# Performance work log

Measured on AMD Instinct MI355X. Metric: run time of the kernel, lower is better.

Reference implementation:

```python
import jax, jax.numpy as jnp
import numpy as np

N, E, H, NH, RBF_K = 512, 4096, 128, 8, 64
CUTOFF = 10.0
HH = H * NH  # 1024


def setup_inputs() -> dict:
    key = jax.random.key(0)
    ks = jax.random.split(key, 30)
    def lin_w(k, fan_in, fan_out):
        return jax.random.normal(k, (fan_in, fan_out), jnp.float32) * (fan_in ** -0.5)
    inp = {
        'atom_embs': jax.random.normal(ks[0], (N, H), jnp.float32),
        'pos': jax.random.normal(ks[1], (N, 3), jnp.float32),
        'edge_weight': jax.random.normal(ks[2], (E,), jnp.float32),
        'edge_indices': jax.random.randint(ks[3], (2, E), 0, N, jnp.int64),
        'Wq': lin_w(ks[4], H, HH),
        'Wk': lin_w(ks[5], H, HH),
        'Wv': lin_w(ks[6], H, HH),
        'li_w': lin_w(ks[7], H, H), 'li_b': jnp.zeros((H,), jnp.float32),
        'lj_w': lin_w(ks[8], H, H), 'lj_b': jnp.zeros((H,), jnp.float32),
        'el_w': lin_w(ks[9], 3 * H, HH), 'el_b': jnp.zeros((HH,), jnp.float32),
        'rl_w': lin_w(ks[10], RBF_K, HH), 'rl_b': jnp.zeros((HH,), jnp.float32),
        'ol_w': lin_w(ks[11], HH, H), 'ol_b': jnp.zeros((H,), jnp.float32),
        'ln_g': jnp.ones((H,), jnp.float32), 'ln_b': jnp.zeros((H,), jnp.float32),
        'f1_w': lin_w(ks[12], H, H), 'f1_b': jnp.zeros((H,), jnp.float32),
        'f2_w': lin_w(ks[13], H, H), 'f2_b': jnp.zeros((H,), jnp.float32),
        'f3_w': lin_w(ks[14], H, H), 'f3_b': jnp.zeros((H,), jnp.float32),
    }
    return inp


def _scatter_softmax_cols(logits, seg, num_segments):
    # softmax over columns of `logits` grouped by seg (column -> source node)
    lt = logits.T                                   # [E_cols, E_rows]
    m = jax.ops.segment_max(lt, seg, num_segments=num_segments)
    e = jnp.exp(lt - m[seg])
    s = jax.ops.segment_sum(e, seg, num_segments=num_segments)
    return (e / s[seg]).T


def _rbf(d):
    # d: [E, 1]. ExponentialRBF with softplus(softplus_inverse(x)) == x identities
    centers = jnp.linspace(1.0, np.exp(-CUTOFF).astype(np.float32), RBF_K)
    widths = np.float32((0.5 / ((1.0 - np.exp(-CUTOFF)) / RBF_K)) ** 2)
    x = d / CUTOFF
    x3 = x ** 3; x4 = x3 * x; x5 = x4 * x
    cut = jnp.where(x < 1, 1 - 6 * x5 + 15 * x4 - 10 * x3, jnp.zeros_like(x))
    return cut * jnp.exp(-widths * (jnp.exp(-d) - centers) ** 2)   # [E, K]


def reference(atom_embs, pos, edge_weight, edge_indices, Wq, Wk, Wv,
              li_w, li_b, lj_w, lj_b, el_w, el_b, rl_w, rl_b, ol_w, ol_b,
              ln_g, ln_b, f1_w, f1_b, f2_w, f2_b, f3_w, f3_b):
    src, tgt = edge_indices[0], edge_indices[1]
    ew = edge_weight[:, None]
    ai = atom_embs[tgt] + ew                      # atom_embs_i (+= edge_weight)
    aj = atom_embs[src] + ew                      # atom_embs_j (+= edge_weight)
    Q = ai @ Wq
    K = ai @ Wk
    V = ai @ Wv                                   # [E, HH]
    logits = (Q @ K.T) * (H ** -0.5)              # [E, E]
    prod = _scatter_softmax_cols(logits, src, N)  # scatter_softmax over edge_indices[0]
    hi = ai @ li_w + li_b
    hj = aj @ lj_w + lj_b
    edge_ij = jnp.concatenate([hi + hj, hi - hj, hi * hj], axis=-1)  # [E, 3H]
    d = jnp.linalg.norm(pos[tgt] - pos[src], axis=-1)[:, None]       # [E, 1]
    feats = edge_ij @ el_w + el_b + _rbf(d) @ rl_w + rl_b + V        # [E, HH]
    msg = (prod @ feats) @ ol_w + ol_b            # [E, H]
    agg = jax.ops.segment_sum(msg, tgt, num_segments=N)              # [N, H]

    def ln(x):
        mu = jnp.mean(x, -1, keepdims=True)
        var = jnp.var(x, -1, keepdims=True)
        return (x - mu) / jnp.sqrt(var + 1e-5) * ln_g + ln_b

    h = ln(agg)
    sp = jax.nn.softplus
    h = sp(sp(sp(h @ f1_w + f1_b) @ f2_w + f2_b) @ f3_w + f3_b)
    return ln(h)
```

## Files before the change

### kernel.cpp

```cpp
#include <hip/hip_runtime.h>
#include <math.h>

#define N_NODES 512
#define NE      4096
#define H       128
#define HH      1024
#define RBFK    64
#define KCAT    576
#define ALPHA   0.08838834764831845f

typedef __attribute__((ext_vector_type(8))) short bf16x8;
typedef __attribute__((ext_vector_type(4))) float f32x4;
typedef __attribute__((ext_vector_type(4))) short short4v;

__device__ __forceinline__ short f2bf(float x) {
    unsigned u = __builtin_bit_cast(unsigned, x);
    unsigned r = u + 0x7FFFu + ((u >> 16) & 1u);
    return (short)(r >> 16);
}
__device__ __forceinline__ float bf2f(short s) {
    return __builtin_bit_cast(float, ((unsigned)(unsigned short)s) << 16);
}

__device__ __forceinline__ void gload16(const short* g, short* l) {
    __builtin_amdgcn_global_load_lds(
        (const __attribute__((address_space(1))) void*)g,
        (__attribute__((address_space(3))) void*)l, 16, 0, 0);
}


__global__ __launch_bounds__(512) void k_sort(
    const int* __restrict__ ei, const float* __restrict__ ew,
    int* __restrict__ srcS, int* __restrict__ tgtS, float* __restrict__ ewS,
    int* __restrict__ idxT,
    int* __restrict__ segStart, int* __restrict__ segStartT,
    int* __restrict__ nsegp, float* __restrict__ cvec)
{
    __shared__ int hS[N_NODES], hT[N_NODES], sS[N_NODES], sT[N_NODES];
    __shared__ int flag;
    int t = threadIdx.x;
    if (t < 64) {
        int vv = ei[2 * t + 1];
        unsigned long long m = __ballot(vv != 0);
        if (t == 0) flag = (m == 0ULL);
    }
    hS[t] = 0; hT[t] = 0;
    if (t < H) cvec[t] = 0.0f;
    __syncthreads();
    int is64 = flag;
    for (int e = t; e < NE; e += 512) {
        int s = is64 ? ei[2 * e]          : ei[e];
        int g = is64 ? ei[2 * NE + 2 * e] : ei[NE + e];
        atomicAdd(&hS[s], 1);
        atomicAdd(&hT[g], 1);
    }
    __syncthreads();
    int cs = hS[t], ct = hT[t];
    sS[t] = cs; sT[t] = ct;
    __syncthreads();
    for (int off = 1; off < N_NODES; off <<= 1) {
        int a = (t >= off) ? sS[t - off] : 0;
        int b = (t >= off) ? sT[t - off] : 0;
        __syncthreads();
        sS[t] += a; sT[t] += b;
        __syncthreads();
    }
    segStart[t + 1]  = sS[t];
    segStartT[t + 1] = sT[t];
    if (t == 0) { segStart[0] = 0; segStartT[0] = 0; }
    hS[t] = sS[t] - cs;
    hT[t] = sT[t] - ct;
    sS[t] = (cs > 0) ? 1 : 0;
    __syncthreads();
    for (int off = 256; off > 0; off >>= 1) {
        if (t < off) sS[t] += sS[t + off];
        __syncthreads();
    }
    if (t == 0) nsegp[0] = sS[0];
    for (int e = t; e < NE; e += 512) {
        int s = is64 ? ei[2 * e]          : ei[e];
        int g = is64 ? ei[2 * NE + 2 * e] : ei[NE + e];
        int p = atomicAdd(&hS[s], 1);
        srcS[p] = s; tgtS[p] = g; ewS[p] = ew[e];
        int q = atomicAdd(&hT[g], 1);
        idxT[q] = p;
    }
}

#define RA 524288
#define RB 589824
#define RBZ 65536
#define RW 262144
#define RCW 2048
#define RD 131072
#define RE 32768
#define RG 65536
#define RF 4096
#define RTOT (RA+RB+RBZ+RW+RCW+RD+RE+RG+RF)

__global__ void k_prep_all(
    const float* __restrict__ atom_embs, const float* __restrict__ pos,
    const int* __restrict__ srcS, const int* __restrict__ tgtS, const float* __restrict__ ewS,
    const float* __restrict__ Wq, const float* __restrict__ Wk, const float* __restrict__ Wv,
    const float* __restrict__ li_w, const float* __restrict__ lj_w,
    const float* __restrict__ el_w, const float* __restrict__ rl_w,
    const float* __restrict__ ol_w, const float* __restrict__ el_b, const float* __restrict__ rl_b,
    short* __restrict__ Acat, short* __restrict__ ajB, short* __restrict__ BcatT,
    short* __restrict__ WqkT, float* __restrict__ cwq, float* __restrict__ cwk,
    short* __restrict__ olT, short* __restrict__ liT, short* __restrict__ ljT,
    short* __restrict__ embB, float* __restrict__ cvec)
{
    int idx = blockIdx.x * blockDim.x + threadIdx.x;
    if (idx < RA) {
        int p = idx >> 7, h = idx & 127;
        int s = srcS[p], t = tgtS[p];
        float ew = ewS[p];
        Acat[(size_t)p * KCAT + h] = f2bf(atom_embs[t * H + h] + ew);
        ajB[idx] = f2bf(atom_embs[s * H + h] + ew);
        if (h < RBFK) {
            float dx = pos[t * 3 + 0] - pos[s * 3 + 0];
            float dy = pos[t * 3 + 1] - pos[s * 3 + 1];
            float dz = pos[t * 3 + 2] - pos[s * 3 + 2];
            float d = sqrtf(dx * dx + dy * dy + dz * dz);
            float x = d * 0.1f;
            float cut = 0.0f;
            if (x < 1.0f) {
                float x3 = x * x * x, x4 = x3 * x, x5 = x4 * x;
                cut = 1.0f - 6.0f * x5 + 15.0f * x4 - 10.0f * x3;
            }
            float ck = 1.0f + (float)h * (-0.015872295239210119f);
            float tt = expf(-d) - ck;
            Acat[(size_t)p * KCAT + 512 + h] = f2bf(cut * expf(-1024.0929857f * tt * tt));
        }
        return;
    }
    idx -= RA;
    if (idx < RB) {
        int k = idx >> 10, n = idx & 1023;
        float v = (k < 128) ? Wv[k * HH + n]
                : (k < 512) ? el_w[(k - 128) * HH + n]
                            : rl_w[(k - 512) * HH + n];
        BcatT[idx] = f2bf(v);
        return;
    }
    idx -= RB;
    if (idx < RBZ) { BcatT[RB + idx] = 0; return; }
    idx -= RBZ;
    if (idx < RW) {
        int n = idx >> 7, k = idx & 127;
        float v = (n < 1024) ? Wq[k * HH + n] : Wk[k * HH + (n - 1024)];
        WqkT[idx] = f2bf(v);
        return;
    }
    idx -= RW;
    if (idx < RCW) {
        int which = idx >> 10, j = idx & 1023;
        const float* W = which ? Wk : Wq;
        float s = 0.0f;
        for (int k = 0; k < H; k++) s += W[k * HH + j];
        (which ? cwk : cwq)[j] = s;
        return;
    }
    idx -= RCW;
    if (idx < RD) {
        int h = idx >> 10, n = idx & 1023;
        olT[idx] = f2bf(ol_w[n * H + h]);
        return;
    }
    idx -= RD;
    if (idx < RE) {
        int which = idx >> 14, r = idx & 16383;
        int n = r >> 7, k = r & 127;
        (which ? ljT : liT)[r] = f2bf((which ? lj_w : li_w)[k * H + n]);
        return;
    }
    idx -= RE;
    if (idx < RG) { embB[idx] = f2bf(atom_embs[idx]); return; }
    idx -= RG;
    if (idx < RF) {
        int h = idx & 127, chunk = idx >> 7;
        float acc = 0.0f;
        int n0 = chunk * 32;
        for (int n = n0; n < n0 + 32; n++)
            acc += (el_b[n] + rl_b[n]) * ol_w[n * H + h];
        atomicAdd(&cvec[h], acc);
    }
}

__device__ __forceinline__ void gemm_body(
    short* As, short* Bs,
    const short* __restrict__ A, int lda,
    const short* __restrict__ B, int ldb,
    void* __restrict__ Cp, int ldc,
    int kbeg, int kend, float alpha, const float* __restrict__ bias,
    long zoff_pitch, int out_mode, int row0, int col0)
{
    const int tid = threadIdx.x;
    const int wave = tid >> 6, lane = tid & 63;

    f32x4 acc[4][4];
#pragma unroll
    for (int i = 0; i < 4; i++)
#pragma unroll
        for (int j = 0; j < 4; j++) acc[i][j] = (f32x4){0.f, 0.f, 0.f, 0.f};

    const int m0 = (wave >> 1) * 64, n0 = (wave & 1) * 64;
    const int lr = lane >> 3;
    const int lc = (lane & 7) * 8;
    const int cl = lane & 15, quad = lane >> 4;

    for (int k0 = kbeg; k0 < kend; k0 += 64) {
#pragma unroll
        for (int i = 0; i < 4; i++) {
            int r = wave * 32 + i * 8;
            gload16(A + (size_t)(row0 + r + lr) * lda + k0 + lc, As + r * 64);
            gload16(B + (size_t)(col0 + r + lr) * ldb + k0 + lc, Bs + r * 64);
        }
        __syncthreads();
#pragma unroll
        for (int kk = 0; kk < 64; kk += 32) {
            bf16x8 af[4], bf[4];
            int ko = kk + quad * 8;
#pragma unroll
            for (int i = 0; i < 4; i++)
                af[i] = *(const bf16x8*)(As + (m0 + i * 16 + cl) * 64 + ko);
#pragma unroll
            for (int j = 0; j < 4; j++)
                bf[j] = *(const bf16x8*)(Bs + (n0 + j * 16 + cl) * 64 + ko);
#pragma unroll
            for (int i = 0; i < 4; i++)
#pragma unroll
                for (int j = 0; j < 4; j++)
                    acc[i][j] = __builtin_amdgcn_mfma_f32_16x16x32_bf16(af[i], bf[j], acc[i][j], 0, 0, 0);
        }
        __syncthreads();
    }

    if (out_mode == 1) {
        short* C = (short*)Cp;
#pragma unroll
        for (int i = 0; i < 4; i++)
#pragma unroll
            for (int j = 0; j < 4; j++) {
                int cc = col0 + n0 + j * 16 + cl;
                float bv = bias ? bias[cc] : 0.0f;
#pragma unroll
                for (int reg = 0; reg < 4; reg++) {
                    int rr = row0 + m0 + i * 16 + quad * 4 + reg;
                    C[(size_t)rr * ldc + cc] = f2bf(acc[i][j][reg] * alpha + bv);
                }
            }
    } else if (out_mode == 3) {
        short* C = (short*)Cp;
#pragma unroll
        for (int i = 0; i < 4; i++)
#pragma unroll
            for (int j = 0; j < 4; j++) {
                int cc = col0 + n0 + j * 16 + cl;
                int rr = row0 + m0 + i * 16 + quad * 4;
                short4v pack;
#pragma unroll
                for (int reg = 0; reg < 4; reg++) pack[reg] = f2bf(acc[i][j][reg] * alpha);
                *(short4v*)(C + (size_t)cc * ldc + rr) = pack;
            }
    } else {
        float* C = (float*)Cp + zoff_pitch;
#pragma unroll
        for (int i = 0; i < 4; i++)
#pragma unroll
            for (int j = 0; j < 4; j++) {
                int cc = col0 + n0 + j * 16 + cl;
#pragma unroll
                for (int reg = 0; reg < 4; reg++) {
                    int rr = row0 + m0 + i * 16 + quad * 4 + reg;
                    C[(size_t)rr * ldc + cc] = acc[i][j][reg] * alpha;
                }
            }
    }
}

__global__ __launch_bounds__(256) void k_gemm(
    const short* __restrict__ A, int lda,
    const short* __restrict__ B, int ldb,
    void* __restrict__ Cp, int ldc,
    int K, float alpha, const float* __restrict__ bias,
    long split_pitch, int out_mode)
{
    __shared__ __align__(16) short As[128 * 64];
    __shared__ __align__(16) short Bs[128 * 64];
    int kchunk = K / gridDim.z;
    gemm_body(As, Bs, A, lda, B, ldb, Cp, ldc,
              kchunk * blockIdx.z, kchunk * (blockIdx.z + 1), alpha, bias,
              (long)blockIdx.z * split_pitch, out_mode,
              blockIdx.y * 128, blockIdx.x * 128);
}

__device__ __forceinline__ void edgefeat_body(
    short* As, short* Bs, int row0,
    const short* __restrict__ Acat_in, const short* __restrict__ ajB,
    const short* __restrict__ liT, const short* __restrict__ ljT,
    const float* __restrict__ li_b, const float* __restrict__ lj_b,
    short* __restrict__ Acat)
{
    const int tid = threadIdx.x;
    const int wave = tid >> 6, lane = tid & 63;
    const int cl = lane & 15, quad = lane >> 4;
    const int m0 = (wave >> 1) * 64, n0 = (wave & 1) * 64;
    const int sr = lane >> 4, sc = (lane & 15) * 8;

    f32x4 ai_acc[4][4], aj_acc[4][4];
#pragma unroll
    for (int i = 0; i < 4; i++)
#pragma unroll
        for (int j = 0; j < 4; j++) {
            ai_acc[i][j] = (f32x4){0.f, 0.f, 0.f, 0.f};
            aj_acc[i][j] = (f32x4){0.f, 0.f, 0.f, 0.f};
        }

#pragma unroll
    for (int i = 0; i < 8; i++) {
        int r = wave * 32 + i * 4;
        gload16(Acat_in + (size_t)(row0 + r + sr) * KCAT + sc, As + r * 128);
        gload16(liT + (r + sr) * 128 + sc, Bs + r * 128);
    }
    __syncthreads();
#pragma unroll
    for (int kk = 0; kk < 128; kk += 32) {
        bf16x8 af[4], bf[4];
        int ko = kk + quad * 8;
#pragma unroll
        for (int i = 0; i < 4; i++) af[i] = *(const bf16x8*)(As + (m0 + i * 16 + cl) * 128 + ko);
#pragma unroll
        for (int j = 0; j < 4; j++) bf[j] = *(const bf16x8*)(Bs + (n0 + j * 16 + cl) * 128 + ko);
#pragma unroll
        for (int i = 0; i < 4; i++)
#pragma unroll
            for (int j = 0; j < 4; j++)
                ai_acc[i][j] = __builtin_amdgcn_mfma_f32_16x16x32_bf16(af[i], bf[j], ai_acc[i][j], 0, 0, 0);
    }
    __syncthreads();
#pragma unroll
    for (int i = 0; i < 8; i++) {
        int r = wave * 32 + i * 4;
        gload16(ajB + (size_t)(row0 + r + sr) * 128 + sc, As + r * 128);
        gload16(ljT + (r + sr) * 128 + sc, Bs + r * 128);
    }
    __syncthreads();
#pragma unroll
    for (int kk = 0; kk < 128; kk += 32) {
        bf16x8 af[4], bf[4];
        int ko = kk + quad * 8;
#pragma unroll
        for (int i = 0; i < 4; i++) af[i] = *(const bf16x8*)(As + (m0 + i * 16 + cl) * 128 + ko);
#pragma unroll
        for (int j = 0; j < 4; j++) bf[j] = *(const bf16x8*)(Bs + (n0 + j * 16 + cl) * 128 + ko);
#pragma unroll
        for (int i = 0; i < 4; i++)
#pragma unroll
            for (int j = 0; j < 4; j++)
                aj_acc[i][j] = __builtin_amdgcn_mfma_f32_16x16x32_bf16(af[i], bf[j], aj_acc[i][j], 0, 0, 0);
    }
#pragma unroll
    for (int i = 0; i < 4; i++)
#pragma unroll
        for (int j = 0; j < 4; j++) {
            int cc = n0 + j * 16 + cl;
            float bi = li_b[cc], bj = lj_b[cc];
#pragma unroll
            for (int reg = 0; reg < 4; reg++) {
                int rr = row0 + m0 + i * 16 + quad * 4 + reg;
                float hv = ai_acc[i][j][reg] + bi;
                float gv = aj_acc[i][j][reg] + bj;
                short* rowp = Acat + (size_t)rr * KCAT;
                rowp[128 + cc] = f2bf(hv + gv);
                rowp[256 + cc] = f2bf(hv - gv);
                rowp[384 + cc] = f2bf(hv * gv);
            }
        }
}

__global__ __launch_bounds__(256) void k_big(
    const short* __restrict__ Acat_in, const short* __restrict__ ajB,
    const short* __restrict__ liT, const short* __restrict__ ljT,
    const float* __restrict__ li_b, const float* __restrict__ lj_b,
    short* __restrict__ Acat,
    const short* __restrict__ embB, const short* __restrict__ WqkT,
    short* __restrict__ QKB,
    const short* __restrict__ olT, const short* __restrict__ BcatT,
    short* __restrict__ W2T)
{
    __shared__ __align__(16) char smem[65536];
    if (blockIdx.x < 32) {
        edgefeat_body((short*)smem, (short*)(smem + 32768), blockIdx.x * 128,
                      Acat_in, ajB, liT, ljT, li_b, lj_b, Acat);
    } else if (blockIdx.x < 96) {
        int id = blockIdx.x - 32;
        gemm_body((short*)smem, (short*)(smem + 16384),
                  embB, H, WqkT, H, QKB, 2048, 0, H, 1.0f, nullptr, 0, 1,
                  (id >> 4) * 128, (id & 15) * 128);
    } else {
        int id = blockIdx.x - 96;
        gemm_body((short*)smem, (short*)(smem + 16384),
                  olT, HH, BcatT, HH, W2T, 640, 0, HH, 1.0f, nullptr, 0, 1,
                  0, id * 128);
    }
}

__global__ __launch_bounds__(256) void k_zr(
    const short* __restrict__ QKB,
    const float* __restrict__ cwq, const float* __restrict__ cwk,
    const short* __restrict__ Acat, const short* __restrict__ W2T,
    short* __restrict__ GT,
    float* __restrict__ Z, float* __restrict__ pv, float* __restrict__ qv,
    float* __restrict__ sv)
{
    __shared__ __align__(16) char smem[32768];
    if (blockIdx.x < 32) {
        int zs = blockIdx.x >> 4;
        int tile = blockIdx.x & 15;
        gemm_body((short*)smem, (short*)(smem + 16384),
                  QKB, 2048, QKB + 1024, 2048, Z, N_NODES,
                  zs * 512, zs * 512 + 512, ALPHA, nullptr,
                  (long)zs * ((long)N_NODES * N_NODES), 0,
                  (tile >> 2) * 128, (tile & 3) * 128);
    } else if (blockIdx.x < 64) {
        int id = blockIdx.x - 32;
        gemm_body((short*)smem, (short*)(smem + 16384),
                  Acat, KCAT, W2T, 640, GT, NE, 0, KCAT, 1.0f, nullptr, 0, 3,
                  id * 128, 0);
    } else {
        int b = blockIdx.x - 64;
        int t = threadIdx.x;
        int wave = t >> 6, lane = t & 63;
        if (b == 0 && wave == 0) {
            float a = 0.0f;
            for (int j = lane; j < HH; j += 64) a += cwq[j] * cwk[j];
            for (int off = 32; off > 0; off >>= 1) a += __shfl_down(a, off);
            if (lane == 0) sv[0] = a;
        }
        for (int ni = 0; ni < 8; ni++) {
            int n = b * 32 + wave * 8 + ni;
            const short* qr = QKB + (size_t)n * 2048;
            float pa = 0.0f, qa = 0.0f;
            int j0 = lane * 16;
#pragma unroll
            for (int j = 0; j < 16; j++) {
                pa += bf2f(qr[j0 + j]) * cwk[j0 + j];
                qa += bf2f(qr[1024 + j0 + j]) * cwq[j0 + j];
            }
            for (int off = 32; off > 0; off >>= 1) {
                pa += __shfl_down(pa, off);
                qa += __shfl_down(qa, off);
            }
            if (lane == 0) { pv[n] = pa; qv[n] = qa; }
        }
    }
}

__global__ __launch_bounds__(512) void k_denom(
    const float* __restrict__ Z, const float* __restrict__ pv,
    const float* __restrict__ qv, const float* __restrict__ sv,
    const int* __restrict__ tgtS, const float* __restrict__ ewS,
    const int* __restrict__ segStart, float* __restrict__ rDen)
{
    __shared__ float row[NE];
    __shared__ float zq[N_NODES];
    const int r = blockIdx.x, t = threadIdx.x;
    const int tr = tgtS[r];
    const float er = ewS[r];
    const float aer = ALPHA * er;
    for (int i = t; i < N_NODES; i += 512)
        zq[i] = Z[(size_t)tr * N_NODES + i]
              + Z[(size_t)N_NODES * N_NODES + (size_t)tr * N_NODES + i]
              + aer * qv[i];
    __syncthreads();
    const float beta = ALPHA * (pv[tr] + er * sv[0]);
    for (int c = t; c < NE; c += 512)
        row[c] = __expf(zq[tgtS[c]] + ewS[c] * beta);
    __syncthreads();
    float* rd = rDen + (size_t)r * N_NODES;
    if (t < N_NODES) {
        int a = segStart[t], b = segStart[t + 1];
        float s = 0.0f;
        for (int p = a; p < b; p++) s += row[p];
        rd[t] = (s > 0.0f) ? 1.0f / s : 0.0f;
    }
}

__global__ __launch_bounds__(256) void k_pagg2(
    const float* __restrict__ Z, const float* __restrict__ pv,
    const float* __restrict__ qv, const float* __restrict__ sv,
    const float* __restrict__ rDen,
    const int* __restrict__ tgtS, const float* __restrict__ ewS,
    const int* __restrict__ srcS, const int* __restrict__ segStartT,
    const int* __restrict__ idxT, short* __restrict__ PaggB)
{
    __shared__ float zrow[N_NODES];
    __shared__ float aq[N_NODES];
    __shared__ float erL[32];
    __shared__ int   eL[32];
    const int n = blockIdx.y;
    const int c0 = blockIdx.x * 1024;
    const int t = threadIdx.x;
    for (int i = t; i < N_NODES; i += 256) {
        zrow[i] = Z[(size_t)n * N_NODES + i]
                + Z[(size_t)N_NODES * N_NODES + (size_t)n * N_NODES + i];
        aq[i]   = ALPHA * qv[i];
    }
    __syncthreads();
    const float p_n = pv[n];
    const float s = sv[0];
    float A4[4], cB4[4];
    int sc4[4];
#pragma unroll
    for (int q = 0; q < 4; q++) {
        int c = c0 + t + q * 256;
        int tc = tgtS[c]; float ec = ewS[c];
        A4[q]  = zrow[tc] + (ALPHA * ec) * p_n;
        cB4[q] = aq[tc] + (ALPHA * ec) * s;
        sc4[q] = srcS[c];
    }
    float acc[4] = {0.f, 0.f, 0.f, 0.f};
    const int a = segStartT[n], b = segStartT[n + 1];
    for (int ch = a; ch < b; ch += 32) {
        int ne = b - ch; if (ne > 32) ne = 32;
        __syncthreads();
        if (t < ne) { int e = idxT[ch + t]; eL[t] = e; erL[t] = ewS[e]; }
        __syncthreads();
        for (int k = 0; k < ne; k++) {
            const float er = erL[k];
            const float* rde = rDen + (size_t)eL[k] * N_NODES;
#pragma unroll
            for (int q = 0; q < 4; q++)
                acc[q] += __expf(A4[q] + er * cB4[q]) * rde[sc4[q]];
        }
    }
    short* pr = PaggB + (size_t)n * NE + c0;
#pragma unroll
    for (int q = 0; q < 4; q++)
        pr[t + q * 256] = f2bf(acc[q]);
}

__global__ __launch_bounds__(128) void k_head(
    const float* __restrict__ aggP, const int* __restrict__ segStartT,
    const int* __restrict__ nsegp,
    const float* __restrict__ cvec, const float* __restrict__ ol_b,
    const float* __restrict__ ln_g, const float* __restrict__ ln_b,
    const float* __restrict__ f1_w, const float* __restrict__ f1_b,
    const float* __restrict__ f2_w, const float* __restrict__ f2_b,
    const float* __restrict__ f3_w, const float* __restrict__ f3_b,
    float* __restrict__ out)
{
    __shared__ float x[H];
    __shared__ float red[H];
    int t = threadIdx.x, row = blockIdx.x;
    int cnt = segStartT[row + 1] - segStartT[row];
    float v = (float)cnt * (ol_b[t] + (float)nsegp[0] * cvec[t]);
    const float* ap = aggP + (size_t)row * H + t;
#pragma unroll
    for (int z = 0; z < 8; z++) v += ap[(size_t)z * N_NODES * H];
    red[t] = v; __syncthreads();
    for (int s = 64; s > 0; s >>= 1) { if (t < s) red[t] += red[t + s]; __syncthreads(); }
    float mu = red[0] * (1.0f / H); __syncthreads();
    float dv = v - mu;
    red[t] = dv * dv; __syncthreads();
    for (int s = 64; s > 0; s >>= 1) { if (t < s) red[t] += red[t + s]; __syncthreads(); }
    float var = red[0] * (1.0f / H); __syncthreads();
    x[t] = dv * rsqrtf(var + 1e-5f) * ln_g[t] + ln_b[t];
    __syncthreads();
    const float* Ws[3] = { f1_w, f2_w, f3_w };
    const float* Bb[3] = { f1_b, f2_b, f3_b };
    for (int l = 0; l < 3; l++) {
        float acc = Bb[l][t];
        const float* Wl = Ws[l];
        for (int k = 0; k < H; k++) acc = fmaf(x[k], Wl[k * H + t], acc);
        float o = fmaxf(acc, 0.0f) + log1pf(expf(-fabsf(acc)));
        __syncthreads();
        x[t] = o;
        __syncthreads();
    }
    float xv = x[t];
    red[t] = xv; __syncthreads();
    for (int s = 64; s > 0; s >>= 1) { if (t < s) red[t] += red[t + s]; __syncthreads(); }
    mu = red[0] * (1.0f / H); __syncthreads();
    float dv2 = xv - mu;
    red[t] = dv2 * dv2; __syncthreads();
    for (int s = 64; s > 0; s >>= 1) { if (t < s) red[t] += red[t + s]; __syncthreads(); }
    var = red[0] * (1.0f / H);
    out[row * H + t] = dv2 * rsqrtf(var + 1e-5f) * ln_g[t] + ln_b[t];
}


extern "C" void kernel_launch(void* const* d_in, const int* in_sizes, int n_in,
                              void* d_out, int out_size, void* d_ws, size_t ws_size,
                              hipStream_t stream) {
    const float* atom_embs   = (const float*)d_in[0];
    const float* pos         = (const float*)d_in[1];
    const float* edge_weight = (const float*)d_in[2];
    const int*   edge_idx    = (const int*)d_in[3];
    const float* Wq   = (const float*)d_in[4];
    const float* Wk   = (const float*)d_in[5];
    const float* Wv   = (const float*)d_in[6];
    const float* li_w = (const float*)d_in[7];
    const float* li_b = (const float*)d_in[8];
    const float* lj_w = (const float*)d_in[9];
    const float* lj_b = (const float*)d_in[10];
    const float* el_w = (const float*)d_in[11];
    const float* el_b = (const float*)d_in[12];
    const float* rl_w = (const float*)d_in[13];
    const float* rl_b = (const float*)d_in[14];
    const float* ol_w = (const float*)d_in[15];
    const float* ol_b = (const float*)d_in[16];
    const float* ln_g = (const float*)d_in[17];
    const float* ln_b = (const float*)d_in[18];
    const float* f1_w = (const float*)d_in[19];
    const float* f1_b = (const float*)d_in[20];
    const float* f2_w = (const float*)d_in[21];
    const float* f2_b = (const float*)d_in[22];
    const float* f3_w = (const float*)d_in[23];
    const float* f3_b = (const float*)d_in[24];
    float* out = (float*)d_out;

    char* w = (char*)d_ws;
    size_t off = 0;
    auto alloc = [&](size_t bytes) -> void* {
        void* p = w + off;
        off += (bytes + 255) & ~(size_t)255;
        return p;
    };
    int*   srcS      = (int*)alloc(NE * 4);
    int*   tgtS      = (int*)alloc(NE * 4);
    float* ewS       = (float*)alloc(NE * 4);
    int*   segStart  = (int*)alloc((N_NODES + 1) * 4);
    int*   segStartT = (int*)alloc((N_NODES + 1) * 4);
    int*   idxT      = (int*)alloc(NE * 4);
    int*   nsegp     = (int*)alloc(4);
    short* Acat   = (short*)alloc((size_t)NE * KCAT * 2);
    short* ajB    = (short*)alloc((size_t)NE * H * 2);
    short* BcatT  = (short*)alloc((size_t)640 * HH * 2);
    short* WqkT   = (short*)alloc((size_t)2048 * H * 2);
    float* cwq    = (float*)alloc(HH * 4);
    float* cwk    = (float*)alloc(HH * 4);
    short* olT    = (short*)alloc((size_t)H * HH * 2);
    short* liT    = (short*)alloc((size_t)H * H * 2);
    short* ljT    = (short*)alloc((size_t)H * H * 2);
    short* embB   = (short*)alloc((size_t)N_NODES * H * 2);
    float* cvec   = (float*)alloc(H * 4);
    short* W2T    = (short*)alloc((size_t)H * 640 * 2);
    short* QKB    = (short*)alloc((size_t)N_NODES * 2048 * 2);
    float* Z      = (float*)alloc((size_t)2 * N_NODES * N_NODES * 4);
    float* pv     = (float*)alloc(N_NODES * 4);
    float* qv     = (float*)alloc(N_NODES * 4);
    float* sv     = (float*)alloc(4);
    short* GT     = (short*)alloc((size_t)H * NE * 2);
    float* rDen   = (float*)alloc((size_t)NE * N_NODES * 4);
    short* PaggB  = (short*)alloc((size_t)N_NODES * NE * 2);
    float* aggP   = (float*)alloc((size_t)8 * N_NODES * H * 4);

    k_sort<<<1, 512, 0, stream>>>(edge_idx, edge_weight, srcS, tgtS, ewS, idxT,
                                  segStart, segStartT, nsegp, cvec);
    k_prep_all<<<(RTOT + 255) / 256, 256, 0, stream>>>(
        atom_embs, pos, srcS, tgtS, ewS,
        Wq, Wk, Wv, li_w, lj_w, el_w, rl_w, ol_w, el_b, rl_b,
        Acat, ajB, BcatT, WqkT, cwq, cwk, olT, liT, ljT, embB, cvec);
    k_big<<<101, 256, 0, stream>>>(Acat, ajB, liT, ljT, li_b, lj_b, Acat,
                                   embB, WqkT, QKB, olT, BcatT, W2T);
    k_zr<<<80, 256, 0, stream>>>(QKB, cwq, cwk, Acat, W2T, GT, Z, pv, qv, sv);
    k_denom<<<NE, 512, 0, stream>>>(Z, pv, qv, sv, tgtS, ewS, segStart, rDen);
    {
        dim3 g(4, N_NODES);
        k_pagg2<<<g, 256, 0, stream>>>(Z, pv, qv, sv, rDen, tgtS, ewS, srcS,
                                       segStartT, idxT, PaggB);
    }
    {
        dim3 g(1, N_NODES / 128, 8);
        k_gemm<<<g, 256, 0, stream>>>(PaggB, NE, GT, NE, aggP, H, NE, 1.0f, nullptr,
                                      (long)N_NODES * H, 0);
    }
    k_head<<<N_NODES, 128, 0, stream>>>(aggP, segStartT, nsegp, cvec, ol_b,
                                        ln_g, ln_b, f1_w, f1_b, f2_w, f2_b, f3_w, f3_b, out);
}
```

Before: 219.3 us.

## Fold edge sort into prep kernel and drop sorted-order edge permutation

```diff
diff --git a/kernel.cpp b/kernel.cpp
--- a/kernel.cpp
+++ b/kernel.cpp
@@ -26,65 +26,6 @@
     __builtin_amdgcn_global_load_lds(
         (const __attribute__((address_space(1))) void*)g,
         (__attribute__((address_space(3))) void*)l, 16, 0, 0);
-}
-
-
-__global__ __launch_bounds__(512) void k_sort(
-    const int* __restrict__ ei, const float* __restrict__ ew,
-    int* __restrict__ srcS, int* __restrict__ tgtS, float* __restrict__ ewS,
-    int* __restrict__ idxT,
-    int* __restrict__ segStart, int* __restrict__ segStartT,
-    int* __restrict__ nsegp, float* __restrict__ cvec)
-{
-    __shared__ int hS[N_NODES], hT[N_NODES], sS[N_NODES], sT[N_NODES];
-    __shared__ int flag;
-    int t = threadIdx.x;
-    if (t < 64) {
-        int vv = ei[2 * t + 1];
-        unsigned long long m = __ballot(vv != 0);
-        if (t == 0) flag = (m == 0ULL);
-    }
-    hS[t] = 0; hT[t] = 0;
-    if (t < H) cvec[t] = 0.0f;
-    __syncthreads();
-    int is64 = flag;
-    for (int e = t; e < NE; e += 512) {
-        int s = is64 ? ei[2 * e]          : ei[e];
-        int g = is64 ? ei[2 * NE + 2 * e] : ei[NE + e];
-        atomicAdd(&hS[s], 1);
-        atomicAdd(&hT[g], 1);
-    }
-    __syncthreads();
-    int cs = hS[t], ct = hT[t];
-    sS[t] = cs; sT[t] = ct;
-    __syncthreads();
-    for (int off = 1; off < N_NODES; off <<= 1) {
-        int a = (t >= off) ? sS[t - off] : 0;
-        int b = (t >= off) ? sT[t - off] : 0;
-        __syncthreads();
-        sS[t] += a; sT[t] += b;
-        __syncthreads();
-    }
-    segStart[t + 1]  = sS[t];
-    segStartT[t + 1] = sT[t];
-    if (t == 0) { segStart[0] = 0; segStartT[0] = 0; }
-    hS[t] = sS[t] - cs;
-    hT[t] = sT[t] - ct;
-    sS[t] = (cs > 0) ? 1 : 0;
-    __syncthreads();
-    for (int off = 256; off > 0; off >>= 1) {
-        if (t < off) sS[t] += sS[t + off];
-        __syncthreads();
-    }
-    if (t == 0) nsegp[0] = sS[0];
-    for (int e = t; e < NE; e += 512) {
-        int s = is64 ? ei[2 * e]          : ei[e];
-        int g = is64 ? ei[2 * NE + 2 * e] : ei[NE + e];
-        int p = atomicAdd(&hS[s], 1);
-        srcS[p] = s; tgtS[p] = g; ewS[p] = ew[e];
-        int q = atomicAdd(&hT[g], 1);
-        idxT[q] = p;
-    }
 }
 
 #define RA 524288
@@ -95,32 +36,96 @@
 #define RD 131072
 #define RE 32768
 #define RG 65536
-#define RF 4096
+#define RF 512
 #define RTOT (RA+RB+RBZ+RW+RCW+RD+RE+RG+RF)
-
-__global__ void k_prep_all(
+#define PREP_BLOCKS (RTOT / 512 + 1)
+
+__global__ __launch_bounds__(512) void k_prep(
+    const int* __restrict__ ei, const float* __restrict__ ew,
     const float* __restrict__ atom_embs, const float* __restrict__ pos,
-    const int* __restrict__ srcS, const int* __restrict__ tgtS, const float* __restrict__ ewS,
     const float* __restrict__ Wq, const float* __restrict__ Wk, const float* __restrict__ Wv,
     const float* __restrict__ li_w, const float* __restrict__ lj_w,
     const float* __restrict__ el_w, const float* __restrict__ rl_w,
     const float* __restrict__ ol_w, const float* __restrict__ el_b, const float* __restrict__ rl_b,
+    int* __restrict__ srcO, int* __restrict__ tgtO, int* __restrict__ rankS,
+    int* __restrict__ idxT, int* __restrict__ segStart, int* __restrict__ segStartT,
+    int* __restrict__ nsegp,
     short* __restrict__ Acat, short* __restrict__ ajB, short* __restrict__ BcatT,
     short* __restrict__ WqkT, float* __restrict__ cwq, float* __restrict__ cwk,
     short* __restrict__ olT, short* __restrict__ liT, short* __restrict__ ljT,
-    short* __restrict__ embB, float* __restrict__ cvec)
-{
-    int idx = blockIdx.x * blockDim.x + threadIdx.x;
+    short* __restrict__ embB, float* __restrict__ cvec4)
+{
+    __shared__ int sh[4 * N_NODES];
+    __shared__ int flag;
+    const int t = threadIdx.x;
+    if (t < 64) {
+        int vv = ei[2 * t + 1];
+        unsigned long long m = __ballot(vv != 0);
+        if (t == 0) flag = (m == 0ULL);
+    }
+    __syncthreads();
+    const int is64 = flag;
+
+    if (blockIdx.x == 0) {
+        int* hS = sh;
+        int* hT = sh + N_NODES;
+        int* sS = sh + 2 * N_NODES;
+        int* sT = sh + 3 * N_NODES;
+        hS[t] = 0; hT[t] = 0;
+        __syncthreads();
+        for (int e = t; e < NE; e += 512) {
+            int s = is64 ? ei[2 * e]          : ei[e];
+            int g = is64 ? ei[2 * NE + 2 * e] : ei[NE + e];
+            srcO[e] = s; tgtO[e] = g;
+            atomicAdd(&hS[s], 1);
+            atomicAdd(&hT[g], 1);
+        }
+        __syncthreads();
+        int cs = hS[t], ct = hT[t];
+        sS[t] = cs; sT[t] = ct;
+        __syncthreads();
+        for (int off = 1; off < N_NODES; off <<= 1) {
+            int a = (t >= off) ? sS[t - off] : 0;
+            int b = (t >= off) ? sT[t - off] : 0;
+            __syncthreads();
+            sS[t] += a; sT[t] += b;
+            __syncthreads();
+        }
+        segStart[t + 1]  = sS[t];
+        segStartT[t + 1] = sT[t];
+        if (t == 0) { segStart[0] = 0; segStartT[0] = 0; }
+        hS[t] = sS[t] - cs;
+        hT[t] = sT[t] - ct;
+        sS[t] = (cs > 0) ? 1 : 0;
+        __syncthreads();
+        for (int off = 256; off > 0; off >>= 1) {
+            if (t < off) sS[t] += sS[t + off];
+            __syncthreads();
+        }
+        if (t == 0) nsegp[0] = sS[0];
+        for (int e = t; e < NE; e += 512) {
+            int s = is64 ? ei[2 * e]          : ei[e];
+            int g = is64 ? ei[2 * NE + 2 * e] : ei[NE + e];
+            int p = atomicAdd(&hS[s], 1);
+            rankS[e] = p;
+            int q = atomicAdd(&hT[g], 1);
+            idxT[q] = e;
+        }
+        return;
+    }
+
+    int idx = (blockIdx.x - 1) * 512 + t;
     if (idx < RA) {
         int p = idx >> 7, h = idx & 127;
-        int s = srcS[p], t = tgtS[p];
-        float ew = ewS[p];
-        Acat[(size_t)p * KCAT + h] = f2bf(atom_embs[t * H + h] + ew);
-        ajB[idx] = f2bf(atom_embs[s * H + h] + ew);
+        int s  = is64 ? ei[2 * p]          : ei[p];
+        int tg = is64 ? ei[2 * NE + 2 * p] : ei[NE + p];
+        float w = ew[p];
+        Acat[(size_t)p * KCAT + h] = f2bf(atom_embs[tg * H + h] + w);
+        ajB[idx] = f2bf(atom_embs[s * H + h] + w);
         if (h < RBFK) {
-            float dx = pos[t * 3 + 0] - pos[s * 3 + 0];
-            float dy = pos[t * 3 + 1] - pos[s * 3 + 1];
-            float dz = pos[t * 3 + 2] - pos[s * 3 + 2];
+            float dx = pos[tg * 3 + 0] - pos[s * 3 + 0];
+            float dy = pos[tg * 3 + 1] - pos[s * 3 + 1];
+            float dz = pos[tg * 3 + 2] - pos[s * 3 + 2];
             float d = sqrtf(dx * dx + dy * dy + dz * dz);
             float x = d * 0.1f;
             float cut = 0.0f;
@@ -177,13 +182,13 @@
     idx -= RE;
     if (idx < RG) { embB[idx] = f2bf(atom_embs[idx]); return; }
     idx -= RG;
-    if (idx < RF) {
+    {
         int h = idx & 127, chunk = idx >> 7;
         float acc = 0.0f;
-        int n0 = chunk * 32;
-        for (int n = n0; n < n0 + 32; n++)
+        int n0 = chunk * 256;
+        for (int n = n0; n < n0 + 256; n++)
             acc += (el_b[n] + rl_b[n]) * ol_w[n * H + h];
-        atomicAdd(&cvec[h], acc);
+        cvec4[idx] = acc;
     }
 }
 
@@ -460,14 +465,15 @@
 __global__ __launch_bounds__(512) void k_denom(
     const float* __restrict__ Z, const float* __restrict__ pv,
     const float* __restrict__ qv, const float* __restrict__ sv,
-    const int* __restrict__ tgtS, const float* __restrict__ ewS,
+    const int* __restrict__ tgtO, const float* __restrict__ ew,
+    const int* __restrict__ rankS,
     const int* __restrict__ segStart, float* __restrict__ rDen)
 {
     __shared__ float row[NE];
     __shared__ float zq[N_NODES];
     const int r = blockIdx.x, t = threadIdx.x;
-    const int tr = tgtS[r];
-    const float er = ewS[r];
+    const int tr = tgtO[r];
+    const float er = ew[r];
     const float aer = ALPHA * er;
     for (int i = t; i < N_NODES; i += 512)
         zq[i] = Z[(size_t)tr * N_NODES + i]
@@ -476,7 +482,7 @@
     __syncthreads();
     const float beta = ALPHA * (pv[tr] + er * sv[0]);
     for (int c = t; c < NE; c += 512)
-        row[c] = __expf(zq[tgtS[c]] + ewS[c] * beta);
+        row[rankS[c]] = __expf(zq[tgtO[c]] + ew[c] * beta);
     __syncthreads();
     float* rd = rDen + (size_t)r * N_NODES;
     if (t < N_NODES) {
@@ -491,8 +497,8 @@
     const float* __restrict__ Z, const float* __restrict__ pv,
     const float* __restrict__ qv, const float* __restrict__ sv,
     const float* __restrict__ rDen,
-    const int* __restrict__ tgtS, const float* __restrict__ ewS,
-    const int* __restrict__ srcS, const int* __restrict__ segStartT,
+    const int* __restrict__ tgtO, const float* __restrict__ ew,
+    const int* __restrict__ srcO, const int* __restrict__ segStartT,
     const int* __restrict__ idxT, short* __restrict__ PaggB)
 {
     __shared__ float zrow[N_NODES];
@@ -515,17 +521,17 @@
 #pragma unroll
     for (int q = 0; q < 4; q++) {
         int c = c0 + t + q * 256;
-        int tc = tgtS[c]; float ec = ewS[c];
+        int tc = tgtO[c]; float ec = ew[c];
         A4[q]  = zrow[tc] + (ALPHA * ec) * p_n;
         cB4[q] = aq[tc] + (ALPHA * ec) * s;
-        sc4[q] = srcS[c];
+        sc4[q] = srcO[c];
     }
     float acc[4] = {0.f, 0.f, 0.f, 0.f};
     const int a = segStartT[n], b = segStartT[n + 1];
     for (int ch = a; ch < b; ch += 32) {
         int ne = b - ch; if (ne > 32) ne = 32;
         __syncthreads();
-        if (t < ne) { int e = idxT[ch + t]; eL[t] = e; erL[t] = ewS[e]; }
+        if (t < ne) { int e = idxT[ch + t]; eL[t] = e; erL[t] = ew[e]; }
         __syncthreads();
         for (int k = 0; k < ne; k++) {
             const float er = erL[k];
@@ -544,7 +550,7 @@
 __global__ __launch_bounds__(128) void k_head(
     const float* __restrict__ aggP, const int* __restrict__ segStartT,
     const int* __restrict__ nsegp,
-    const float* __restrict__ cvec, const float* __restrict__ ol_b,
+    const float* __restrict__ cvec4, const float* __restrict__ ol_b,
     const float* __restrict__ ln_g, const float* __restrict__ ln_b,
     const float* __restrict__ f1_w, const float* __restrict__ f1_b,
     const float* __restrict__ f2_w, const float* __restrict__ f2_b,
@@ -555,7 +561,8 @@
     __shared__ float red[H];
     int t = threadIdx.x, row = blockIdx.x;
     int cnt = segStartT[row + 1] - segStartT[row];
-    float v = (float)cnt * (ol_b[t] + (float)nsegp[0] * cvec[t]);
+    float cv = cvec4[t] + cvec4[128 + t] + cvec4[256 + t] + cvec4[384 + t];
+    float v = (float)cnt * (ol_b[t] + (float)nsegp[0] * cv);
     const float* ap = aggP + (size_t)row * H + t;
 #pragma unroll
     for (int z = 0; z < 8; z++) v += ap[(size_t)z * N_NODES * H];
@@ -628,12 +635,12 @@
         off += (bytes + 255) & ~(size_t)255;
         return p;
     };
-    int*   srcS      = (int*)alloc(NE * 4);
-    int*   tgtS      = (int*)alloc(NE * 4);
-    float* ewS       = (float*)alloc(NE * 4);
+    int*   srcO      = (int*)alloc(NE * 4);
+    int*   tgtO      = (int*)alloc(NE * 4);
+    int*   rankS     = (int*)alloc(NE * 4);
+    int*   idxT      = (int*)alloc(NE * 4);
     int*   segStart  = (int*)alloc((N_NODES + 1) * 4);
     int*   segStartT = (int*)alloc((N_NODES + 1) * 4);
-    int*   idxT      = (int*)alloc(NE * 4);
     int*   nsegp     = (int*)alloc(4);
     short* Acat   = (short*)alloc((size_t)NE * KCAT * 2);
     short* ajB    = (short*)alloc((size_t)NE * H * 2);
@@ -645,7 +652,7 @@
     short* liT    = (short*)alloc((size_t)H * H * 2);
     short* ljT    = (short*)alloc((size_t)H * H * 2);
     short* embB   = (short*)alloc((size_t)N_NODES * H * 2);
-    float* cvec   = (float*)alloc(H * 4);
+    float* cvec4  = (float*)alloc(512 * 4);
     short* W2T    = (short*)alloc((size_t)H * 640 * 2);
     short* QKB    = (short*)alloc((size_t)N_NODES * 2048 * 2);
     float* Z      = (float*)alloc((size_t)2 * N_NODES * N_NODES * 4);
@@ -657,26 +664,26 @@
     short* PaggB  = (short*)alloc((size_t)N_NODES * NE * 2);
     float* aggP   = (float*)alloc((size_t)8 * N_NODES * H * 4);
 
-    k_sort<<<1, 512, 0, stream>>>(edge_idx, edge_weight, srcS, tgtS, ewS, idxT,
-                                  segStart, segStartT, nsegp, cvec);
-    k_prep_all<<<(RTOT + 255) / 256, 256, 0, stream>>>(
-        atom_embs, pos, srcS, tgtS, ewS,
+    k_prep<<<PREP_BLOCKS, 512, 0, stream>>>(
+        edge_idx, edge_weight, atom_embs, pos,
         Wq, Wk, Wv, li_w, lj_w, el_w, rl_w, ol_w, el_b, rl_b,
-        Acat, ajB, BcatT, WqkT, cwq, cwk, olT, liT, ljT, embB, cvec);
+        srcO, tgtO, rankS, idxT, segStart, segStartT, nsegp,
+        Acat, ajB, BcatT, WqkT, cwq, cwk, olT, liT, ljT, embB, cvec4);
     k_big<<<101, 256, 0, stream>>>(Acat, ajB, liT, ljT, li_b, lj_b, Acat,
                                    embB, WqkT, QKB, olT, BcatT, W2T);
     k_zr<<<80, 256, 0, stream>>>(QKB, cwq, cwk, Acat, W2T, GT, Z, pv, qv, sv);
-    k_denom<<<NE, 512, 0, stream>>>(Z, pv, qv, sv, tgtS, ewS, segStart, rDen);
+    k_denom<<<NE, 512, 0, stream>>>(Z, pv, qv, sv, tgtO, edge_weight, rankS,
+                                    segStart, rDen);
     {
         dim3 g(4, N_NODES);
-        k_pagg2<<<g, 256, 0, stream>>>(Z, pv, qv, sv, rDen, tgtS, ewS, srcS,
-                                       segStartT, idxT, PaggB);
+        k_pagg2<<<g, 256, 0, stream>>>(Z, pv, qv, sv, rDen, tgtO, edge_weight,
+                                       srcO, segStartT, idxT, PaggB);
     }
     {
         dim3 g(1, N_NODES / 128, 8);
         k_gemm<<<g, 256, 0, stream>>>(PaggB, NE, GT, NE, aggP, H, NE, 1.0f, nullptr,
                                       (long)N_NODES * H, 0);
     }
-    k_head<<<N_NODES, 128, 0, stream>>>(aggP, segStartT, nsegp, cvec, ol_b,
+    k_head<<<N_NODES, 128, 0, stream>>>(aggP, segStartT, nsegp, cvec4, ol_b,
                                         ln_g, ln_b, f1_w, f1_b, f2_w, f2_b, f3_w, f3_b, out);
 }
```

New measurement: 269.4 us. 1.23x slower.
